# Performance work log

Measured on AMD Instinct MI355X. Metric: run time of the kernel, lower is better.

## Reference

```python
import jax, jax.numpy as jnp
import numpy as np

MARGIN = 0.5
N_CLASSES = 100

def setup_inputs() -> dict:
    key = jax.random.key(0)
    k1, k2 = jax.random.split(key)
    n, d = 8192, 128
    inputs = jax.random.normal(k1, (n, d), dtype=jnp.float32)
    targets = jax.random.randint(k2, (n,), 0, N_CLASSES, dtype=jnp.int64)
    return {"inputs": inputs, "targets": targets}

def reference(inputs, targets):
    # pairwise squared euclidean distances: [n, n]
    sq = jnp.sum(inputs * inputs, axis=1)  # [n]
    dist = sq[:, None] + sq[None, :] - 2.0 * (inputs @ inputs.T)
    dist = jnp.maximum(dist, 0.0)
    # positive mask: same label (diagonal included, matching original)
    mask = targets[:, None] == targets[None, :]  # [n, n] bool
    big = jnp.float32(1e30)
    dist_ap = jnp.max(jnp.where(mask, dist, -big), axis=1)  # hardest positive per row
    dist_an = jnp.min(jnp.where(mask, big, dist), axis=1)   # hardest negative per row
    loss = jnp.sum(jax.nn.relu(dist_ap - dist_an + MARGIN))
    return loss
```

## Files before the change

### kernel.cpp

```cpp
#include <hip/hip_runtime.h>
#include <hip/hip_bf16.h>

#define D 128
#define MARGIN 0.5f
#define LDB 136

typedef __attribute__((ext_vector_type(8))) short bf16x8;
typedef __attribute__((ext_vector_type(4))) float f32x4;

__global__ void prep_kernel(const float* __restrict__ x,
                            float* __restrict__ sq,
                            unsigned* __restrict__ ap,
                            unsigned* __restrict__ an,
                            __hip_bfloat16* __restrict__ xb,
                            float* __restrict__ out, int n) {
    int tid = threadIdx.x;
    int row = blockIdx.x * 4 + (tid >> 6);
    int lane = tid & 63;
    const float2* xr = (const float2*)(x + (size_t)row * D);
    float2 v = xr[lane];
    __hip_bfloat162 b2;
    b2.x = __float2bfloat16(v.x);
    b2.y = __float2bfloat16(v.y);
    ((__hip_bfloat162*)(xb + (size_t)row * D))[lane] = b2;
    float s = v.x * v.x + v.y * v.y;
    #pragma unroll
    for (int o = 32; o > 0; o >>= 1) s += __shfl_xor(s, o, 64);
    if (lane == 0) {
        sq[row] = s;
        ap[row] = 0u;
        an[row] = 0x7F800000u;
    }
    if (blockIdx.x == 0 && tid == 0) *out = 0.0f;
}

__launch_bounds__(256, 2)
__global__ void gram_kernel(const __hip_bfloat16* __restrict__ xb,
                            const float* __restrict__ sq,
                            const int* __restrict__ tgt,
                            unsigned* __restrict__ ap,
                            unsigned* __restrict__ an, int n) {
    __shared__ __align__(16) __hip_bfloat16 Asb[128 * LDB];
    __shared__ __align__(16) __hip_bfloat16 Bsb[128 * LDB];
    __shared__ float sqB[128];
    __shared__ int   tgtB[128];

    const int tid  = threadIdx.x;
    const int wid  = tid >> 6;
    const int lane = tid & 63;
    const int quad = lane >> 4;
    const int l    = lane & 15;
    const int w_mi = wid >> 1;
    const int w_nj = wid & 1;
    const int i0   = blockIdx.x * 128;

    {
        const float4* src = (const float4*)(xb + (size_t)i0 * D);
        #pragma unroll
        for (int it = 0; it < 8; ++it) {
            int cid = it * 256 + tid;
            int r = cid >> 4, c = cid & 15;
            *(float4*)(&Asb[r * LDB + c * 8]) = src[r * 16 + c];
        }
    }
    __syncthreads();

    bf16x8 afrag[4][4];
    #pragma unroll
    for (int mt = 0; mt < 4; ++mt) {
        int r = w_mi * 64 + mt * 16 + l;
        #pragma unroll
        for (int ks = 0; ks < 4; ++ks)
            afrag[mt][ks] = *(const bf16x8*)(&Asb[r * LDB + ks * 32 + quad * 8]);
    }

    int li[4][4];
    #pragma unroll
    for (int mt = 0; mt < 4; ++mt)
        #pragma unroll
        for (int reg = 0; reg < 4; ++reg)
            li[mt][reg] = tgt[i0 + w_mi * 64 + mt * 16 + quad * 4 + reg];

    float lap[4][4], lan[4][4];
    #pragma unroll
    for (int mt = 0; mt < 4; ++mt)
        #pragma unroll
        for (int reg = 0; reg < 4; ++reg) { lap[mt][reg] = -1e30f; lan[mt][reg] = 1e30f; }

    for (int jj = 0; jj < 8; ++jj) {
        const int j0 = (blockIdx.y * 8 + jj) * 128;
        __syncthreads();
        {
            const float4* src = (const float4*)(xb + (size_t)j0 * D);
            #pragma unroll
            for (int it = 0; it < 8; ++it) {
                int cid = it * 256 + tid;
                int r = cid >> 4, c = cid & 15;
                *(float4*)(&Bsb[r * LDB + c * 8]) = src[r * 16 + c];
            }
            if (tid < 128) { sqB[tid] = sq[j0 + tid]; tgtB[tid] = tgt[j0 + tid]; }
        }
        __syncthreads();

        float sjv[4]; int tjv[4];
        #pragma unroll
        for (int jt = 0; jt < 4; ++jt) {
            int c = w_nj * 64 + jt * 16 + l;
            sjv[jt] = sqB[c]; tjv[jt] = tgtB[c];
        }

        f32x4 acc[4][4];
        #pragma unroll
        for (int mt = 0; mt < 4; ++mt)
            #pragma unroll
            for (int jt = 0; jt < 4; ++jt)
                acc[mt][jt] = (f32x4){0.f, 0.f, 0.f, 0.f};

        #pragma unroll
        for (int ks = 0; ks < 4; ++ks) {
            bf16x8 bfr[4];
            #pragma unroll
            for (int jt = 0; jt < 4; ++jt) {
                int r = w_nj * 64 + jt * 16 + l;
                bfr[jt] = *(const bf16x8*)(&Bsb[r * LDB + ks * 32 + quad * 8]);
            }
            #pragma unroll
            for (int mt = 0; mt < 4; ++mt)
                #pragma unroll
                for (int jt = 0; jt < 4; ++jt)
                    acc[mt][jt] = __builtin_amdgcn_mfma_f32_16x16x32_bf16(
                        afrag[mt][ks], bfr[jt], acc[mt][jt], 0, 0, 0);
        }

        #pragma unroll
        for (int mt = 0; mt < 4; ++mt)
            #pragma unroll
            for (int jt = 0; jt < 4; ++jt)
                #pragma unroll
                for (int reg = 0; reg < 4; ++reg) {
                    float t = fmaf(-2.0f, acc[mt][jt][reg], sjv[jt]);
                    bool same = (li[mt][reg] == tjv[jt]);
                    lap[mt][reg] = fmaxf(lap[mt][reg], same ? t : -1e30f);
                    lan[mt][reg] = fminf(lan[mt][reg], same ? 1e30f : t);
                }
    }

    #pragma unroll
    for (int mt = 0; mt < 4; ++mt)
        #pragma unroll
        for (int reg = 0; reg < 4; ++reg) {
            float p = lap[mt][reg], q = lan[mt][reg];
            #pragma unroll
            for (int o = 1; o < 16; o <<= 1) {
                p = fmaxf(p, __shfl_xor(p, o, 64));
                q = fminf(q, __shfl_xor(q, o, 64));
            }
            if (l == mt * 4 + reg) {
                int gi = i0 + w_mi * 64 + mt * 16 + quad * 4 + reg;
                float s = sq[gi];
                atomicMax(&ap[gi], __float_as_uint(fmaxf(s + p, 0.0f)));
                atomicMin(&an[gi], __float_as_uint(fmaxf(s + q, 0.0f)));
            }
        }
}

__global__ void final_kernel(const unsigned* __restrict__ ap,
                             const unsigned* __restrict__ an,
                             float* __restrict__ out, int n) {
    int i = blockIdx.x * blockDim.x + threadIdx.x;
    float v = 0.f;
    if (i < n) {
        float p = __uint_as_float(ap[i]);
        float q = __uint_as_float(an[i]);
        v = fmaxf(p - q + MARGIN, 0.0f);
    }
    #pragma unroll
    for (int o = 32; o > 0; o >>= 1) v += __shfl_xor(v, o, 64);
    __shared__ float ws[4];
    int lane = threadIdx.x & 63, w = threadIdx.x >> 6;
    if (lane == 0) ws[w] = v;
    __syncthreads();
    if (threadIdx.x == 0) atomicAdd(out, ws[0] + ws[1] + ws[2] + ws[3]);
}

extern "C" void kernel_launch(void* const* d_in, const int* in_sizes, int n_in,
                              void* d_out, int out_size, void* d_ws, size_t ws_size,
                              hipStream_t stream) {
    const float* x   = (const float*)d_in[0];
    const int*   tgt = (const int*)d_in[1];
    float* out = (float*)d_out;
    const int n = in_sizes[1];

    float*          sq = (float*)d_ws;
    unsigned*       ap = (unsigned*)((char*)d_ws + (size_t)n * 4);
    unsigned*       an = ap + n;
    __hip_bfloat16* xb = (__hip_bfloat16*)((char*)d_ws + (size_t)n * 12);

    prep_kernel<<<n / 4, 256, 0, stream>>>(x, sq, ap, an, xb, out, n);
    dim3 grid(n / 128, 8);
    gram_kernel<<<grid, 256, 0, stream>>>(xb, sq, tgt, ap, an, n);
    final_kernel<<<n / 256, 256, 0, stream>>>(ap, an, out, n);
}
```

Before: 91.15 us.

## Drop LDS staging; each wave streams B fragments from global with register double-buffering

The gram kernel no longer stages A and B tiles in shared memory. Each wave independently owns a 64-row strip and a 512-column split, loading A fragments and 16-column B chunks straight from global memory into registers, with a two-deep software pipeline so the next chunk's load overlaps the current MFMAs. This removes __syncthreads and LDS traffic, at the cost of lower per-wave data reuse (4 MFMAs per B load instead of 16) and more global/L2 traffic.

```diff
diff --git a/kernel.cpp b/kernel.cpp
--- a/kernel.cpp
+++ b/kernel.cpp
@@ -3,7 +3,8 @@
 
 #define D 128
 #define MARGIN 0.5f
-#define LDB 136
+#define NSPLIT 16
+#define NCHUNK 32
 
 typedef __attribute__((ext_vector_type(8))) short bf16x8;
 typedef __attribute__((ext_vector_type(4))) float f32x4;
@@ -40,38 +41,25 @@
                             const int* __restrict__ tgt,
                             unsigned* __restrict__ ap,
                             unsigned* __restrict__ an, int n) {
-    __shared__ __align__(16) __hip_bfloat16 Asb[128 * LDB];
-    __shared__ __align__(16) __hip_bfloat16 Bsb[128 * LDB];
-    __shared__ float sqB[128];
-    __shared__ int   tgtB[128];
-
     const int tid  = threadIdx.x;
     const int wid  = tid >> 6;
     const int lane = tid & 63;
     const int quad = lane >> 4;
     const int l    = lane & 15;
-    const int w_mi = wid >> 1;
-    const int w_nj = wid & 1;
-    const int i0   = blockIdx.x * 128;
-
-    {
-        const float4* src = (const float4*)(xb + (size_t)i0 * D);
-        #pragma unroll
-        for (int it = 0; it < 8; ++it) {
-            int cid = it * 256 + tid;
-            int r = cid >> 4, c = cid & 15;
-            *(float4*)(&Asb[r * LDB + c * 8]) = src[r * 16 + c];
-        }
-    }
-    __syncthreads();
+    const int gw     = blockIdx.x * 4 + wid;
+    const int istrip = gw >> 4;
+    const int jsplit = gw & 15;
+    const int i0 = istrip * 64;
+    const int j0 = jsplit * (16 * NCHUNK);
 
     bf16x8 afrag[4][4];
-    #pragma unroll
-    for (int mt = 0; mt < 4; ++mt) {
-        int r = w_mi * 64 + mt * 16 + l;
+    {
+        const __hip_bfloat16* abase = xb + (size_t)(i0 + l) * D + quad * 8;
         #pragma unroll
-        for (int ks = 0; ks < 4; ++ks)
-            afrag[mt][ks] = *(const bf16x8*)(&Asb[r * LDB + ks * 32 + quad * 8]);
+        for (int mt = 0; mt < 4; ++mt)
+            #pragma unroll
+            for (int ks = 0; ks < 4; ++ks)
+                afrag[mt][ks] = *(const bf16x8*)(abase + (size_t)mt * 16 * D + ks * 32);
     }
 
     int li[4][4];
@@ -79,84 +67,74 @@
     for (int mt = 0; mt < 4; ++mt)
         #pragma unroll
         for (int reg = 0; reg < 4; ++reg)
-            li[mt][reg] = tgt[i0 + w_mi * 64 + mt * 16 + quad * 4 + reg];
+            li[mt][reg] = tgt[i0 + mt * 16 + quad * 4 + reg];
 
-    float lap[4][4], lan[4][4];
+    float lap[16], lan[16];
     #pragma unroll
-    for (int mt = 0; mt < 4; ++mt)
-        #pragma unroll
-        for (int reg = 0; reg < 4; ++reg) { lap[mt][reg] = -1e30f; lan[mt][reg] = 1e30f; }
+    for (int k = 0; k < 16; ++k) { lap[k] = -1e30f; lan[k] = 1e30f; }
 
-    for (int jj = 0; jj < 8; ++jj) {
-        const int j0 = (blockIdx.y * 8 + jj) * 128;
-        __syncthreads();
-        {
-            const float4* src = (const float4*)(xb + (size_t)j0 * D);
-            #pragma unroll
-            for (int it = 0; it < 8; ++it) {
-                int cid = it * 256 + tid;
-                int r = cid >> 4, c = cid & 15;
-                *(float4*)(&Bsb[r * LDB + c * 8]) = src[r * 16 + c];
-            }
-            if (tid < 128) { sqB[tid] = sq[j0 + tid]; tgtB[tid] = tgt[j0 + tid]; }
-        }
-        __syncthreads();
+    const __hip_bfloat16* bbase = xb + (size_t)(j0 + l) * D + quad * 8;
 
-        float sjv[4]; int tjv[4];
-        #pragma unroll
-        for (int jt = 0; jt < 4; ++jt) {
-            int c = w_nj * 64 + jt * 16 + l;
-            sjv[jt] = sqB[c]; tjv[jt] = tgtB[c];
-        }
+    bf16x8 bf[2][4];
+    float  sj[2];
+    int    tj[2];
 
-        f32x4 acc[4][4];
-        #pragma unroll
-        for (int mt = 0; mt < 4; ++mt)
-            #pragma unroll
-            for (int jt = 0; jt < 4; ++jt)
-                acc[mt][jt] = (f32x4){0.f, 0.f, 0.f, 0.f};
+    #define LOADB(buf, c)                                                   \
+        do {                                                                \
+            const __hip_bfloat16* p_ = bbase + (size_t)(c) * 16 * D;        \
+            bf[buf][0] = *(const bf16x8*)(p_);                              \
+            bf[buf][1] = *(const bf16x8*)(p_ + 32);                         \
+            bf[buf][2] = *(const bf16x8*)(p_ + 64);                         \
+            bf[buf][3] = *(const bf16x8*)(p_ + 96);                         \
+            sj[buf] = sq[j0 + (c) * 16 + l];                                \
+            tj[buf] = tgt[j0 + (c) * 16 + l];                               \
+        } while (0)
 
-        #pragma unroll
-        for (int ks = 0; ks < 4; ++ks) {
-            bf16x8 bfr[4];
-            #pragma unroll
-            for (int jt = 0; jt < 4; ++jt) {
-                int r = w_nj * 64 + jt * 16 + l;
-                bfr[jt] = *(const bf16x8*)(&Bsb[r * LDB + ks * 32 + quad * 8]);
-            }
-            #pragma unroll
-            for (int mt = 0; mt < 4; ++mt)
-                #pragma unroll
-                for (int jt = 0; jt < 4; ++jt)
-                    acc[mt][jt] = __builtin_amdgcn_mfma_f32_16x16x32_bf16(
-                        afrag[mt][ks], bfr[jt], acc[mt][jt], 0, 0, 0);
-        }
+    #define COMPUTE(buf)                                                    \
+        do {                                                                \
+            f32x4 acc[4];                                                   \
+            _Pragma("unroll")                                               \
+            for (int mt = 0; mt < 4; ++mt) acc[mt] = (f32x4){0.f,0.f,0.f,0.f}; \
+            _Pragma("unroll")                                               \
+            for (int ks = 0; ks < 4; ++ks)                                  \
+                _Pragma("unroll")                                           \
+                for (int mt = 0; mt < 4; ++mt)                              \
+                    acc[mt] = __builtin_amdgcn_mfma_f32_16x16x32_bf16(      \
+                        afrag[mt][ks], bf[buf][ks], acc[mt], 0, 0, 0);      \
+            float sjc = sj[buf]; int tjc = tj[buf];                         \
+            _Pragma("unroll")                                               \
+            for (int mt = 0; mt < 4; ++mt)                                  \
+                _Pragma("unroll")                                           \
+                for (int reg = 0; reg < 4; ++reg) {                         \
+                    float t = fmaf(-2.0f, acc[mt][reg], sjc);               \
+                    bool same = (li[mt][reg] == tjc);                       \
+                    lap[mt*4+reg] = fmaxf(lap[mt*4+reg], same ? t : -1e30f);\
+                    lan[mt*4+reg] = fminf(lan[mt*4+reg], same ? 1e30f : t); \
+                }                                                           \
+        } while (0)
 
-        #pragma unroll
-        for (int mt = 0; mt < 4; ++mt)
-            #pragma unroll
-            for (int jt = 0; jt < 4; ++jt)
-                #pragma unroll
-                for (int reg = 0; reg < 4; ++reg) {
-                    float t = fmaf(-2.0f, acc[mt][jt][reg], sjv[jt]);
-                    bool same = (li[mt][reg] == tjv[jt]);
-                    lap[mt][reg] = fmaxf(lap[mt][reg], same ? t : -1e30f);
-                    lan[mt][reg] = fminf(lan[mt][reg], same ? 1e30f : t);
-                }
+    LOADB(0, 0);
+    for (int c = 0; c < NCHUNK; c += 2) {
+        LOADB(1, c + 1);
+        COMPUTE(0);
+        if (c < NCHUNK - 2) LOADB(0, c + 2);
+        COMPUTE(1);
     }
+    #undef LOADB
+    #undef COMPUTE
 
     #pragma unroll
     for (int mt = 0; mt < 4; ++mt)
         #pragma unroll
         for (int reg = 0; reg < 4; ++reg) {
-            float p = lap[mt][reg], q = lan[mt][reg];
+            float p = lap[mt*4+reg], q = lan[mt*4+reg];
             #pragma unroll
             for (int o = 1; o < 16; o <<= 1) {
                 p = fmaxf(p, __shfl_xor(p, o, 64));
                 q = fminf(q, __shfl_xor(q, o, 64));
             }
             if (l == mt * 4 + reg) {
-                int gi = i0 + w_mi * 64 + mt * 16 + quad * 4 + reg;
+                int gi = i0 + mt * 16 + quad * 4 + reg;
                 float s = sq[gi];
                 atomicMax(&ap[gi], __float_as_uint(fmaxf(s + p, 0.0f)));
                 atomicMin(&an[gi], __float_as_uint(fmaxf(s + q, 0.0f)));
@@ -197,7 +175,6 @@
     __hip_bfloat16* xb = (__hip_bfloat16*)((char*)d_ws + (size_t)n * 12);
 
     prep_kernel<<<n / 4, 256, 0, stream>>>(x, sq, ap, an, xb, out, n);
-    dim3 grid(n / 128, 8);
-    gram_kernel<<<grid, 256, 0, stream>>>(xb, sq, tgt, ap, an, n);
+    gram_kernel<<<(n / 64) * NSPLIT / 4, 256, 0, stream>>>(xb, sq, tgt, ap, an, n);
     final_kernel<<<n / 256, 256, 0, stream>>>(ap, an, out, n);
 }
```

Result: slower. 103.1 us (+13.1%).
